# Kernel optimization log

Measured on AMD Instinct MI355X. Metric: run time of the kernel, lower is better.

## Reference

```python
import jax, jax.numpy as jnp
import numpy as np

B, NB, NS = 2048, 64, 16          # batch, boxes per tree, symmetry ops per tree
BOX, SYM, F, H = 12, 8, 512, 1024  # boxSize, symmetrySize, featureSize, hiddenSize


def _ops_seq():
    # valid shift-reduce program: shift two leaves, reduce, then (shift, reduce)
    # for the remaining leaves, then apply NS symmetry ops to the root.
    ops = [0, 0, 1]
    for _ in range(NB - 2):
        ops += [0, 1]
    ops += [2] * NS
    return np.array(ops, dtype=np.int64)


def setup_inputs():
    key = jax.random.key(0)
    ks = jax.random.split(key, 12)
    def n(k, shape, s):
        return jax.random.normal(k, shape, dtype=jnp.float32) * s
    return {
        "inputStacks": n(ks[0], (B, NB, BOX), 1.0),
        "symmetryStacks": n(ks[1], (B, NS, SYM), 1.0),
        "operations": jnp.tile(jnp.asarray(_ops_seq())[None, None, :], (B, 1, 1)),
        # BoxEncoder
        "Wb": n(ks[2], (F, BOX), BOX ** -0.5), "bb": jnp.zeros((F,), jnp.float32),
        # AdjEncoder (right linear has no bias, as in the torch module)
        "Wl": n(ks[3], (H, F), F ** -0.5), "bl": jnp.zeros((H,), jnp.float32),
        "Wr": n(ks[4], (H, F), F ** -0.5),
        "Ws": n(ks[5], (F, H), H ** -0.5), "bs": jnp.zeros((F,), jnp.float32),
        # SymEncoder
        "Sl": n(ks[6], (H, F), F ** -0.5), "sbl": jnp.zeros((H,), jnp.float32),
        "Sr": n(ks[7], (H, SYM), SYM ** -0.5), "sbr": jnp.zeros((H,), jnp.float32),
        "Ss": n(ks[8], (F, H), H ** -0.5), "sbs": jnp.zeros((F,), jnp.float32),
    }


def _forward(inputStacks, symmetryStacks, Wb, bb, Wl, bl, Wr, Ws, bs,
             Sl, sbl, Sr, sbr, Ss, sbs, ops_np):
    boxes = jnp.tanh(inputStacks @ Wb.T + bb)  # [B, NB, F]  BoxEncoder
    Bn, nb, f = boxes.shape
    # static max stack depth from the (constant) op schedule
    depth, maxd = 0, 1
    for op in ops_np:
        depth += 1 if op == 0 else (-1 if op == 1 else 0)
        maxd = max(maxd, depth)
    stack = jnp.zeros((Bn, maxd, f), boxes.dtype)
    sp, bp, symp = 0, nb, symmetryStacks.shape[1]
    for op in ops_np:  # same program for every batch element -> fully batched steps
        if op == 0:  # shift: buffers pop from the end (torch list.pop())
            bp -= 1
            stack = stack.at[:, sp].set(boxes[:, bp])
            sp += 1
        elif op == 1:  # adjacency reduce: pop right then left, push result
            left, right = stack[:, sp - 2], stack[:, sp - 1]
            h = jnp.tanh(left @ Wl.T + bl + right @ Wr.T)
            out = jnp.tanh(h @ Ws.T + bs)
            sp -= 1
            stack = stack.at[:, sp - 1].set(out)
        else:  # op == 2: symmetry reduce (pop feature + pop sym param, push)
            symp -= 1
            h = jnp.tanh(stack[:, sp - 1] @ Sl.T + sbl
                         + symmetryStacks[:, symp] @ Sr.T + sbr)
            out = jnp.tanh(h @ Ss.T + sbs)
            stack = stack.at[:, sp - 1].set(out)
    return stack[:, sp - 1]  # [B, F] root codes


def reference(inputStacks, symmetryStacks, operations, Wb, bb, Wl, bl, Wr, Ws, bs,
              Sl, sbl, Sr, sbr, Ss, sbs):
    ops_np = np.asarray(operations)[0, 0]  # identical program across the batch
    return _forward(inputStacks, symmetryStacks, Wb, bb, Wl, bl, Wr, Ws, bs,
                    Sl, sbl, Sr, sbr, Ss, sbs, ops_np)
```

## Files before the change

### kernel.cpp

```cpp
#include <hip/hip_runtime.h>
#include <cmath>

using u16 = unsigned short;
using u32 = unsigned int;
using bf16x8 = __attribute__((ext_vector_type(8))) __bf16;
using f32x4 = __attribute__((ext_vector_type(4))) float;

__device__ __forceinline__ u16 f2bf(float f) {
  union { float f; u32 i; } x; x.f = f;
  u32 r = x.i + 0x7FFFu + ((x.i >> 16) & 1u);
  return (u16)(r >> 16);
}
__device__ __forceinline__ float bf2f(u16 u) {
  union { u32 i; float f; } x; x.i = (u32)u << 16; return x.f;
}

__global__ void cvt_bf16(const float* __restrict__ src, u16* __restrict__ dst, int n) {
  int i = (blockIdx.x * 256 + threadIdx.x) * 8;
  if (i + 8 <= n) {
    float4 a = *(const float4*)(src + i), b = *(const float4*)(src + i + 4);
    u16 t[8] = {f2bf(a.x), f2bf(a.y), f2bf(a.z), f2bf(a.w),
                f2bf(b.x), f2bf(b.y), f2bf(b.z), f2bf(b.w)};
    *(uint4*)(dst + i) = *(uint4*)t;
  }
}

__global__ __launch_bounds__(256) void box_all_v2(const float* __restrict__ inp,
    const float* __restrict__ Wb, const float* __restrict__ bb, u16* __restrict__ boxes) {
  int b = blockIdx.x, t = threadIdx.x;
  __shared__ float sin_[64][12];
  for (int idx = t; idx < 768; idx += 256) sin_[idx / 12][idx % 12] = inp[(long)b * 768 + idx];
  const int f0 = t * 2;
  float w0[12], w1[12];
#pragma unroll
  for (int q = 0; q < 12; ++q) { w0[q] = Wb[f0 * 12 + q]; w1[q] = Wb[(f0 + 1) * 12 + q]; }
  float b0 = bb[f0], b1 = bb[f0 + 1];
  __syncthreads();
  for (int i = 0; i < 64; ++i) {
    float a0 = b0, a1 = b1;
#pragma unroll
    for (int q = 0; q < 12; ++q) { float x = sin_[i][q]; a0 += x * w0[q]; a1 += x * w1[q]; }
    u32 pk = (u32)f2bf(tanhf(a0)) | ((u32)f2bf(tanhf(a1)) << 16);
    *(u32*)&boxes[(((long)b * 64 + i) * 512) + f0] = pk;
  }
}

__global__ void box_one_kernel(const float* __restrict__ inp, const float* __restrict__ Wb,
                               const float* __restrict__ bb, int bp, u16* __restrict__ outBox) {
  int b = blockIdx.x;
  int f = threadIdx.x;
  __shared__ float s_in[12];
  if (f < 12) s_in[f] = inp[((long)b * 64 + bp) * 12 + f];
  __syncthreads();
  float a = bb[f];
#pragma unroll
  for (int q = 0; q < 12; ++q) a += s_in[q] * Wb[f * 12 + q];
  outBox[(long)b * 512 + f] = f2bf(tanhf(a));
}

__global__ __launch_bounds__(256) void gemm64(
    const u16* __restrict__ A1, int lda1,
    const u16* __restrict__ W1b, const float* __restrict__ W1f, int K1,
    const u16* __restrict__ A2, int lda2,
    const u16* __restrict__ W2b, const float* __restrict__ W2f, int K2,
    const float* __restrict__ bias,
    const u16* __restrict__ Radd, long ldr,
    const float* __restrict__ symS, const float* __restrict__ Srw, const float* __restrict__ sbr,
    int doTanh, int outMode, long ldRout,
    u16* __restrict__ Cb, float* __restrict__ Cf, int N) {
  __shared__ u16 As[64][72];
  __shared__ u16 Bs[64][72];
  const int tid = threadIdx.x;
  const int lane = tid & 63, w = tid >> 6;
  const int wr = w >> 1, wc = w & 1;
  const int quad = lane >> 4, l16 = lane & 15;
  const int m0 = blockIdx.y * 64, n0 = blockIdx.x * 64;
  const int srow = tid >> 2, scol = (tid & 3) * 16;

  f32x4 acc[2][2];
#pragma unroll
  for (int i = 0; i < 2; ++i)
#pragma unroll
    for (int j = 0; j < 2; ++j) acc[i][j] = (f32x4){0.f, 0.f, 0.f, 0.f};

#pragma unroll
  for (int pair = 0; pair < 2; ++pair) {
    const u16* A = pair ? A2 : A1;
    const u16* Wb_ = pair ? W2b : W1b;
    const float* Wf_ = pair ? W2f : W1f;
    const int lda = pair ? lda2 : lda1;
    const int K = pair ? K2 : K1;
    if (K == 0) continue;
    for (int k0 = 0; k0 < K; k0 += 64) {
      const u16* ap = &A[(long)(m0 + srow) * lda + k0 + scol];
      uint4 av0 = *(const uint4*)ap;
      uint4 av1 = *(const uint4*)(ap + 8);
      uint4 bv0, bv1;
      if (Wb_) {
        const u16* wp = &Wb_[(long)(n0 + srow) * K + k0 + scol];
        bv0 = *(const uint4*)wp;
        bv1 = *(const uint4*)(wp + 8);
      } else {
        const float* wp = &Wf_[(long)(n0 + srow) * K + k0 + scol];
        u16 t[16];
#pragma unroll
        for (int q = 0; q < 16; ++q) t[q] = f2bf(wp[q]);
        bv0 = ((uint4*)t)[0];
        bv1 = ((uint4*)t)[1];
      }
      __syncthreads();
      *(uint4*)&As[srow][scol] = av0;
      *(uint4*)&As[srow][scol + 8] = av1;
      *(uint4*)&Bs[srow][scol] = bv0;
      *(uint4*)&Bs[srow][scol + 8] = bv1;
      __syncthreads();
      bf16x8 af[2][2], bfv[2][2];
#pragma unroll
      for (int kk = 0; kk < 2; ++kk) {
#pragma unroll
        for (int i = 0; i < 2; ++i)
          af[i][kk] = *(const bf16x8*)&As[wr * 32 + i * 16 + l16][kk * 32 + quad * 8];
#pragma unroll
        for (int j = 0; j < 2; ++j)
          bfv[j][kk] = *(const bf16x8*)&Bs[wc * 32 + j * 16 + l16][kk * 32 + quad * 8];
      }
#pragma unroll
      for (int kk = 0; kk < 2; ++kk)
#pragma unroll
        for (int i = 0; i < 2; ++i)
#pragma unroll
          for (int j = 0; j < 2; ++j)
            acc[i][j] = __builtin_amdgcn_mfma_f32_16x16x32_bf16(af[i][kk], bfv[j][kk], acc[i][j], 0, 0, 0);
    }
  }

#pragma unroll
  for (int j = 0; j < 2; ++j) {
    const int n = n0 + wc * 32 + j * 16 + l16;
    float bn = bias ? bias[n] : 0.0f;
    float srn[8];
    if (symS) {
      bn += sbr[n];
#pragma unroll
      for (int q = 0; q < 8; ++q) srn[q] = Srw[n * 8 + q];
    }
#pragma unroll
    for (int i = 0; i < 2; ++i) {
#pragma unroll
      for (int r = 0; r < 4; ++r) {
        const int m = m0 + wr * 32 + i * 16 + quad * 4 + r;
        float v = acc[i][j][r] + bn;
        if (Radd) v += bf2f(Radd[(long)m * ldr + n]);
        if (symS) {
#pragma unroll
          for (int q = 0; q < 8; ++q) v += symS[(long)m * 128 + q] * srn[q];
        }
        if (doTanh) v = tanhf(v);
        if (outMode == 0) Cb[(long)m * N + n] = f2bf(v);
        else if (outMode == 1) Cf[(long)m * N + n] = v;
        else {
          int ii = m & 63;
          if (ii != 63) Cb[(long)ii * ldRout + (long)(m >> 6) * N + n] = f2bf(v);
        }
      }
    }
  }
}

extern "C" void kernel_launch(void* const* d_in, const int* in_sizes, int n_in,
                              void* d_out, int out_size, void* d_ws, size_t ws_size,
                              hipStream_t stream) {
  const float* inp = (const float*)d_in[0];
  const float* sym = (const float*)d_in[1];
  const float* Wb  = (const float*)d_in[3];
  const float* bb  = (const float*)d_in[4];
  const float* Wl  = (const float*)d_in[5];
  const float* bl  = (const float*)d_in[6];
  const float* Wr  = (const float*)d_in[7];
  const float* Ws  = (const float*)d_in[8];
  const float* bs  = (const float*)d_in[9];
  const float* Sl  = (const float*)d_in[10];
  const float* sbl = (const float*)d_in[11];
  const float* Sr  = (const float*)d_in[12];
  const float* sbr = (const float*)d_in[13];
  const float* Ss  = (const float*)d_in[14];
  const float* sbs = (const float*)d_in[15];

  const long B = 2048, NB = 64, F = 512, H = 1024;
  const long WE = 524288;
  u16* ws = (u16*)d_ws;

  const size_t szW = 5 * WE * 2, szBoxes = (size_t)B * NB * F * 2, szR = (size_t)63 * B * H * 2;
  const size_t szH = (size_t)B * H * 2, szAcc = (size_t)B * F * 2;
  const size_t needT1 = szW + szBoxes + szR + szH + szAcc;
  const size_t needT2 = szW + szBoxes + szH + szAcc;
  const size_t needT3 = szBoxes + szH + szAcc;
  int tier = (ws_size >= needT1) ? 1 : (ws_size >= needT2) ? 2 : (ws_size >= needT3) ? 3 : 4;

  dim3 blk(256);
  dim3 gH(16, 32), gP(8, 32), gR(16, 2048);

  u16 *WlB = nullptr, *WrB = nullptr, *WsB = nullptr, *SlB = nullptr, *SsB = nullptr;
  const float *WlF = Wl, *WrF = Wr, *WsF = Ws, *SlF = Sl, *SsF = Ss;
  u16* p = ws;
  if (tier <= 2) {
    WlB = p; WrB = p + WE; WsB = p + 2 * WE; SlB = p + 3 * WE; SsB = p + 4 * WE;
    p += 5 * WE;
    cvt_bf16<<<WE / 2048, blk, 0, stream>>>(Wl, WlB, (int)WE);
    cvt_bf16<<<WE / 2048, blk, 0, stream>>>(Wr, WrB, (int)WE);
    cvt_bf16<<<WE / 2048, blk, 0, stream>>>(Ws, WsB, (int)WE);
    cvt_bf16<<<WE / 2048, blk, 0, stream>>>(Sl, SlB, (int)WE);
    cvt_bf16<<<WE / 2048, blk, 0, stream>>>(Ss, SsB, (int)WE);
    WlF = WrF = WsF = SlF = SsF = nullptr;
  }

  u16 *accBuf, *hBuf;
  if (tier <= 3) {
    u16* boxes = p;
    p += B * NB * F;
    u16* Rbuf = nullptr;
    if (tier == 1) { Rbuf = p; p += 63 * B * H; }
    hBuf = p; p += B * H;
    accBuf = p;
    box_all_v2<<<B, blk, 0, stream>>>(inp, Wb, bb, boxes);
    if (tier == 1) {
      gemm64<<<gR, blk, 0, stream>>>(boxes, 512, WrB, WrF, 512,
                                     nullptr, 0, nullptr, nullptr, 0,
                                     nullptr, nullptr, 0, nullptr, nullptr, nullptr,
                                     0, 2, B * H, Rbuf, nullptr, 1024);
    }
    const u16* curA = boxes + 63 * 512;
    int curLda = (int)(NB * F);
    for (int bp = 62; bp >= 0; --bp) {
      if (tier == 1) {
        gemm64<<<gH, blk, 0, stream>>>(curA, curLda, WlB, WlF, 512,
                                       nullptr, 0, nullptr, nullptr, 0,
                                       bl, Rbuf + (long)bp * B * H, 1024,
                                       nullptr, nullptr, nullptr, 1, 0, 0, hBuf, nullptr, 1024);
      } else {
        gemm64<<<gH, blk, 0, stream>>>(curA, curLda, WlB, WlF, 512,
                                       boxes + (long)bp * 512, (int)(NB * F), WrB, WrF, 512,
                                       bl, nullptr, 0, nullptr, nullptr, nullptr,
                                       1, 0, 0, hBuf, nullptr, 1024);
      }
      gemm64<<<gP, blk, 0, stream>>>(hBuf, 1024, WsB, WsF, 1024,
                                     nullptr, 0, nullptr, nullptr, 0,
                                     bs, nullptr, 0, nullptr, nullptr, nullptr,
                                     1, 0, 0, accBuf, nullptr, 512);
      curA = accBuf;
      curLda = 512;
    }
  } else {
    u16* box63 = ws;
    u16* boxCur = box63 + B * F;
    hBuf = boxCur + B * F;
    accBuf = hBuf + B * H;
    box_one_kernel<<<B, 512, 0, stream>>>(inp, Wb, bb, 63, box63);
    const u16* curA = box63;
    int curLda = 512;
    for (int bp = 62; bp >= 0; --bp) {
      box_one_kernel<<<B, 512, 0, stream>>>(inp, Wb, bb, bp, boxCur);
      gemm64<<<gH, blk, 0, stream>>>(curA, curLda, nullptr, Wl, 512,
                                     boxCur, 512, nullptr, Wr, 512,
                                     bl, nullptr, 0, nullptr, nullptr, nullptr,
                                     1, 0, 0, hBuf, nullptr, 1024);
      gemm64<<<gP, blk, 0, stream>>>(hBuf, 1024, nullptr, Ws, 1024,
                                     nullptr, 0, nullptr, nullptr, 0,
                                     bs, nullptr, 0, nullptr, nullptr, nullptr,
                                     1, 0, 0, accBuf, nullptr, 512);
      curA = accBuf;
      curLda = 512;
    }
  }

  for (int symp = 15; symp >= 0; --symp) {
    gemm64<<<gH, blk, 0, stream>>>(accBuf, 512, SlB, SlF, 512,
                                   nullptr, 0, nullptr, nullptr, 0,
                                   sbl, nullptr, 0, sym + symp * 8, Sr, sbr,
                                   1, 0, 0, hBuf, nullptr, 1024);
    int om = (symp == 0) ? 1 : 0;
    gemm64<<<gP, blk, 0, stream>>>(hBuf, 1024, SsB, SsF, 1024,
                                   nullptr, 0, nullptr, nullptr, 0,
                                   sbs, nullptr, 0, nullptr, nullptr, nullptr,
                                   1, om, 0, accBuf, (float*)d_out, 512);
  }
  (void)in_sizes; (void)n_in; (void)out_size;
}
```

Baseline: 2.847 ms.

## Fuse sequential tree reduction and symmetry chain into one persistent kernel

Replaces roughly 160 per-step GEMM launches with one persistent chain_kernel. Each block owns 16 batch rows and keeps its activations in LDS across all 79 adjacency and symmetry steps, streaming bf16 weights from global/L2. It also adds a time-major box layout, a dedicated 128x128 GEMM that uses global_load_lds to precompute all right-child products, and an exp-based fast tanh. The trade-off is that only 128 blocks are launched and every step re-reads the full weights per block, which leans on L2 bandwidth; the fast tanh also slightly changes numerics.

```diff
diff --git a/kernel.cpp b/kernel.cpp
--- a/kernel.cpp
+++ b/kernel.cpp
@@ -13,6 +13,14 @@
 }
 __device__ __forceinline__ float bf2f(u16 u) {
   union { u32 i; float f; } x; x.i = (u32)u << 16; return x.f;
+}
+__device__ __forceinline__ float fast_tanh(float x) {
+  float e = __expf(2.0f * x);
+  return 1.0f - 2.0f / (e + 1.0f);
+}
+__device__ __forceinline__ void load_lds16(const u16* g, u16* l) {
+  __builtin_amdgcn_global_load_lds((const __attribute__((address_space(1))) u32*)g,
+                                   (__attribute__((address_space(3))) u32*)l, 16, 0, 0);
 }
 
 __global__ void cvt_bf16(const float* __restrict__ src, u16* __restrict__ dst, int n) {
@@ -25,6 +33,220 @@
   }
 }
 
+__global__ __launch_bounds__(256) void box_allT(const float* __restrict__ inp,
+    const float* __restrict__ Wb, const float* __restrict__ bb, u16* __restrict__ boxesT) {
+  int b = blockIdx.x, t = threadIdx.x;
+  __shared__ float sin_[64][12];
+  for (int idx = t; idx < 768; idx += 256) sin_[idx / 12][idx % 12] = inp[(long)b * 768 + idx];
+  int f0 = (t & 127) * 4, hf = t >> 7;
+  float w[4][12], bz[4];
+#pragma unroll
+  for (int r = 0; r < 4; ++r) {
+    bz[r] = bb[f0 + r];
+#pragma unroll
+    for (int q = 0; q < 12; ++q) w[r][q] = Wb[(f0 + r) * 12 + q];
+  }
+  __syncthreads();
+  for (int i = hf; i < 64; i += 2) {
+    float a[4] = {bz[0], bz[1], bz[2], bz[3]};
+#pragma unroll
+    for (int q = 0; q < 12; ++q) {
+      float x = sin_[i][q];
+#pragma unroll
+      for (int r = 0; r < 4; ++r) a[r] += x * w[r][q];
+    }
+    u16 p[4];
+#pragma unroll
+    for (int r = 0; r < 4; ++r) p[r] = f2bf(fast_tanh(a[r]));
+    *(uint2*)&boxesT[((long)i * 2048 + b) * 512 + f0] = *(uint2*)p;
+  }
+}
+
+__global__ __launch_bounds__(256, 2) void gemm_R(const u16* __restrict__ A,
+                                                 const u16* __restrict__ W,
+                                                 u16* __restrict__ R) {
+  __shared__ u16 smem[8192];
+  const int tid = threadIdx.x, lane = tid & 63, w = tid >> 6;
+  const int wr = w >> 1, wc = w & 1, q = lane >> 4, l16 = lane & 15;
+  const long m0 = (long)blockIdx.y * 128;
+  const int n0 = blockIdx.x * 128;
+  f32x4 C[4][4];
+#pragma unroll
+  for (int i = 0; i < 4; ++i)
+#pragma unroll
+    for (int j = 0; j < 4; ++j) C[i][j] = (f32x4){0.f, 0.f, 0.f, 0.f};
+
+  for (int k0 = 0; k0 < 512; k0 += 32) {
+    __syncthreads();
+#pragma unroll
+    for (int jj = 0; jj < 2; ++jj) {
+      int c = jj * 256 + w * 64;
+      int ch = c + lane;
+      load_lds16(&A[(m0 + (ch >> 2)) * 512 + k0 + (ch & 3) * 8], &smem[0] + c * 8);
+      load_lds16(&W[((long)(n0 + (ch >> 2))) * 512 + k0 + (ch & 3) * 8], &smem[4096] + c * 8);
+    }
+    __syncthreads();
+    bf16x8 af[4], bfv[4];
+#pragma unroll
+    for (int i = 0; i < 4; ++i) af[i] = *(const bf16x8*)&smem[(wr * 64 + i * 16 + l16) * 32 + q * 8];
+#pragma unroll
+    for (int j = 0; j < 4; ++j) bfv[j] = *(const bf16x8*)&smem[4096 + (wc * 64 + j * 16 + l16) * 32 + q * 8];
+#pragma unroll
+    for (int i = 0; i < 4; ++i)
+#pragma unroll
+      for (int j = 0; j < 4; ++j)
+        C[i][j] = __builtin_amdgcn_mfma_f32_16x16x32_bf16(af[i], bfv[j], C[i][j], 0, 0, 0);
+  }
+  for (int hv = 0; hv < 2; ++hv) {
+    __syncthreads();
+    if (wc == hv) {
+#pragma unroll
+      for (int i = 0; i < 4; ++i)
+#pragma unroll
+        for (int j = 0; j < 4; ++j)
+#pragma unroll
+          for (int r = 0; r < 4; ++r)
+            smem[(wr * 64 + i * 16 + q * 4 + r) * 64 + j * 16 + l16] = f2bf(C[i][j][r]);
+    }
+    __syncthreads();
+    u16* dst = R + (m0 + (tid >> 1)) * 1024 + n0 + hv * 64 + (tid & 1) * 32;
+    const u16* s = &smem[(tid >> 1) * 64 + (tid & 1) * 32];
+#pragma unroll
+    for (int v = 0; v < 4; ++v) ((uint4*)dst)[v] = ((const uint4*)s)[v];
+  }
+}
+
+__global__ __launch_bounds__(256, 1) void chain_kernel(
+    const u16* __restrict__ boxesT, const u16* __restrict__ Rbuf,
+    const u16* __restrict__ Wl, const u16* __restrict__ Ws,
+    const u16* __restrict__ Sl, const u16* __restrict__ Ss,
+    const float* __restrict__ bl, const float* __restrict__ bs,
+    const float* __restrict__ sbl, const float* __restrict__ sbr,
+    const float* __restrict__ sbs, const float* __restrict__ SrF,
+    const float* __restrict__ sym, float* __restrict__ outF) {
+  __shared__ u16 sA[16][520];
+  __shared__ u16 sH[16][1032];
+  __shared__ float sSym[16][8];
+
+  const int tid = threadIdx.x, lane = tid & 63, w = tid >> 6;
+  const int q = lane >> 4, l16 = lane & 15;
+  const int m0 = blockIdx.x * 16;
+
+  {
+    const u16* src = boxesT + ((long)63 * 2048 + m0) * 512;
+    int o = tid * 32, r = o >> 9, c = o & 511;
+#pragma unroll
+    for (int v = 0; v < 4; ++v)
+      *(uint4*)&sA[r][c + v * 8] = *(const uint4*)&src[(long)r * 512 + c + v * 8];
+  }
+  __syncthreads();
+
+  for (int t = 0; t < 79; ++t) {
+    const bool symPhase = (t >= 63);
+    const int bp = 62 - t;
+    if (symPhase) {
+      int symp = 15 - (t - 63);
+      if (tid < 128) sSym[tid >> 3][tid & 7] = sym[((long)(m0 + (tid >> 3)) * 16 + symp) * 8 + (tid & 7)];
+      __syncthreads();
+    }
+    const u16* WL = symPhase ? Sl : Wl;
+    u16 rv0[8][4], rv1[8][4];
+    if (!symPhase) {
+      const u16* rbase = Rbuf + ((long)bp * 2048 + m0) * 1024;
+#pragma unroll
+      for (int np = 0; np < 8; ++np) {
+        int nb = w * 256 + np * 32 + l16;
+#pragma unroll
+        for (int r = 0; r < 4; ++r) {
+          rv0[np][r] = rbase[(long)(q * 4 + r) * 1024 + nb];
+          rv1[np][r] = rbase[(long)(q * 4 + r) * 1024 + nb + 16];
+        }
+      }
+    }
+    bf16x8 Af[16];
+#pragma unroll
+    for (int s = 0; s < 16; ++s) Af[s] = *(const bf16x8*)&sA[l16][s * 32 + q * 8];
+    float symv[4][8];
+    if (symPhase) {
+#pragma unroll
+      for (int r = 0; r < 4; ++r)
+#pragma unroll
+        for (int k = 0; k < 8; ++k) symv[r][k] = sSym[q * 4 + r][k];
+    }
+    for (int np = 0; np < 8; ++np) {
+      int n0 = w * 256 + np * 32;
+      f32x4 C0 = {0.f, 0.f, 0.f, 0.f}, C1 = {0.f, 0.f, 0.f, 0.f};
+      const u16* w0 = WL + (long)(n0 + l16) * 512 + q * 8;
+      const u16* w1 = w0 + 16 * 512;
+#pragma unroll 8
+      for (int s = 0; s < 16; ++s) {
+        bf16x8 b0 = *(const bf16x8*)(w0 + s * 32);
+        bf16x8 b1 = *(const bf16x8*)(w1 + s * 32);
+        C0 = __builtin_amdgcn_mfma_f32_16x16x32_bf16(Af[s], b0, C0, 0, 0, 0);
+        C1 = __builtin_amdgcn_mfma_f32_16x16x32_bf16(Af[s], b1, C1, 0, 0, 0);
+      }
+      int n0b = n0 + l16, n1b = n0 + 16 + l16;
+      float bn0, bn1, sr0[8], sr1[8];
+      if (!symPhase) { bn0 = bl[n0b]; bn1 = bl[n1b]; }
+      else {
+        bn0 = sbl[n0b] + sbr[n0b]; bn1 = sbl[n1b] + sbr[n1b];
+        *(float4*)&sr0[0] = *(const float4*)&SrF[(long)n0b * 8];
+        *(float4*)&sr0[4] = *(const float4*)&SrF[(long)n0b * 8 + 4];
+        *(float4*)&sr1[0] = *(const float4*)&SrF[(long)n1b * 8];
+        *(float4*)&sr1[4] = *(const float4*)&SrF[(long)n1b * 8 + 4];
+      }
+#pragma unroll
+      for (int r = 0; r < 4; ++r) {
+        int m = q * 4 + r;
+        float v0 = C0[r] + bn0;
+        float v1 = C1[r] + bn1;
+        if (!symPhase) { v0 += bf2f(rv0[np][r]); v1 += bf2f(rv1[np][r]); }
+        else {
+#pragma unroll
+          for (int k = 0; k < 8; ++k) { v0 += symv[r][k] * sr0[k]; v1 += symv[r][k] * sr1[k]; }
+        }
+        sH[m][n0b] = f2bf(fast_tanh(v0));
+        sH[m][n1b] = f2bf(fast_tanh(v1));
+      }
+    }
+    __syncthreads();
+    const u16* WP = symPhase ? Ss : Ws;
+    const float* b2 = symPhase ? sbs : bs;
+    bf16x8 Hf[32];
+#pragma unroll
+    for (int s = 0; s < 32; ++s) Hf[s] = *(const bf16x8*)&sH[l16][s * 32 + q * 8];
+    const bool last = (t == 78);
+    for (int fp = 0; fp < 4; ++fp) {
+      int f0 = w * 128 + fp * 32;
+      f32x4 C0 = {0.f, 0.f, 0.f, 0.f}, C1 = {0.f, 0.f, 0.f, 0.f};
+      const u16* w0 = WP + (long)(f0 + l16) * 1024 + q * 8;
+      const u16* w1 = w0 + 16 * 1024;
+#pragma unroll 8
+      for (int s = 0; s < 32; ++s) {
+        bf16x8 b0 = *(const bf16x8*)(w0 + s * 32);
+        bf16x8 b1 = *(const bf16x8*)(w1 + s * 32);
+        C0 = __builtin_amdgcn_mfma_f32_16x16x32_bf16(Hf[s], b0, C0, 0, 0, 0);
+        C1 = __builtin_amdgcn_mfma_f32_16x16x32_bf16(Hf[s], b1, C1, 0, 0, 0);
+      }
+      int f0b = f0 + l16, f1b = f0 + 16 + l16;
+      float bn0 = b2[f0b], bn1 = b2[f1b];
+#pragma unroll
+      for (int r = 0; r < 4; ++r) {
+        int m = q * 4 + r;
+        float a0 = fast_tanh(C0[r] + bn0);
+        float a1 = fast_tanh(C1[r] + bn1);
+        sA[m][f0b] = f2bf(a0);
+        sA[m][f1b] = f2bf(a1);
+        if (last) {
+          outF[(long)(m0 + m) * 512 + f0b] = a0;
+          outF[(long)(m0 + m) * 512 + f1b] = a1;
+        }
+      }
+    }
+    __syncthreads();
+  }
+}
+
 __global__ __launch_bounds__(256) void box_all_v2(const float* __restrict__ inp,
     const float* __restrict__ Wb, const float* __restrict__ bb, u16* __restrict__ boxes) {
   int b = blockIdx.x, t = threadIdx.x;
@@ -40,22 +262,9 @@
     float a0 = b0, a1 = b1;
 #pragma unroll
     for (int q = 0; q < 12; ++q) { float x = sin_[i][q]; a0 += x * w0[q]; a1 += x * w1[q]; }
-    u32 pk = (u32)f2bf(tanhf(a0)) | ((u32)f2bf(tanhf(a1)) << 16);
+    u32 pk = (u32)f2bf(fast_tanh(a0)) | ((u32)f2bf(fast_tanh(a1)) << 16);
     *(u32*)&boxes[(((long)b * 64 + i) * 512) + f0] = pk;
   }
-}
-
-__global__ void box_one_kernel(const float* __restrict__ inp, const float* __restrict__ Wb,
-                               const float* __restrict__ bb, int bp, u16* __restrict__ outBox) {
-  int b = blockIdx.x;
-  int f = threadIdx.x;
-  __shared__ float s_in[12];
-  if (f < 12) s_in[f] = inp[((long)b * 64 + bp) * 12 + f];
-  __syncthreads();
-  float a = bb[f];
-#pragma unroll
-  for (int q = 0; q < 12; ++q) a += s_in[q] * Wb[f * 12 + q];
-  outBox[(long)b * 512 + f] = f2bf(tanhf(a));
 }
 
 __global__ __launch_bounds__(256) void gemm64(
@@ -64,9 +273,8 @@
     const u16* __restrict__ A2, int lda2,
     const u16* __restrict__ W2b, const float* __restrict__ W2f, int K2,
     const float* __restrict__ bias,
-    const u16* __restrict__ Radd, long ldr,
     const float* __restrict__ symS, const float* __restrict__ Srw, const float* __restrict__ sbr,
-    int doTanh, int outMode, long ldRout,
+    int doTanh, int outMode,
     u16* __restrict__ Cb, float* __restrict__ Cf, int N) {
   __shared__ u16 As[64][72];
   __shared__ u16 Bs[64][72];
@@ -76,13 +284,11 @@
   const int quad = lane >> 4, l16 = lane & 15;
   const int m0 = blockIdx.y * 64, n0 = blockIdx.x * 64;
   const int srow = tid >> 2, scol = (tid & 3) * 16;
-
   f32x4 acc[2][2];
 #pragma unroll
   for (int i = 0; i < 2; ++i)
 #pragma unroll
     for (int j = 0; j < 2; ++j) acc[i][j] = (f32x4){0.f, 0.f, 0.f, 0.f};
-
 #pragma unroll
   for (int pair = 0; pair < 2; ++pair) {
     const u16* A = pair ? A2 : A1;
@@ -102,11 +308,11 @@
         bv1 = *(const uint4*)(wp + 8);
       } else {
         const float* wp = &Wf_[(long)(n0 + srow) * K + k0 + scol];
-        u16 t[16];
-#pragma unroll
-        for (int q = 0; q < 16; ++q) t[q] = f2bf(wp[q]);
-        bv0 = ((uint4*)t)[0];
-        bv1 = ((uint4*)t)[1];
+        u16 tv[16];
+#pragma unroll
+        for (int qq = 0; qq < 16; ++qq) tv[qq] = f2bf(wp[qq]);
+        bv0 = ((uint4*)tv)[0];
+        bv1 = ((uint4*)tv)[1];
       }
       __syncthreads();
       *(uint4*)&As[srow][scol] = av0;
@@ -133,7 +339,6 @@
             acc[i][j] = __builtin_amdgcn_mfma_f32_16x16x32_bf16(af[i][kk], bfv[j][kk], acc[i][j], 0, 0, 0);
     }
   }
-
 #pragma unroll
   for (int j = 0; j < 2; ++j) {
     const int n = n0 + wc * 32 + j * 16 + l16;
@@ -142,7 +347,7 @@
     if (symS) {
       bn += sbr[n];
 #pragma unroll
-      for (int q = 0; q < 8; ++q) srn[q] = Srw[n * 8 + q];
+      for (int qq = 0; qq < 8; ++qq) srn[qq] = Srw[n * 8 + qq];
     }
 #pragma unroll
     for (int i = 0; i < 2; ++i) {
@@ -150,18 +355,13 @@
       for (int r = 0; r < 4; ++r) {
         const int m = m0 + wr * 32 + i * 16 + quad * 4 + r;
         float v = acc[i][j][r] + bn;
-        if (Radd) v += bf2f(Radd[(long)m * ldr + n]);
         if (symS) {
 #pragma unroll
-          for (int q = 0; q < 8; ++q) v += symS[(long)m * 128 + q] * srn[q];
+          for (int qq = 0; qq < 8; ++qq) v += symS[(long)m * 128 + qq] * srn[qq];
         }
-        if (doTanh) v = tanhf(v);
+        if (doTanh) v = fast_tanh(v);
         if (outMode == 0) Cb[(long)m * N + n] = f2bf(v);
-        else if (outMode == 1) Cf[(long)m * N + n] = v;
-        else {
-          int ii = m & 63;
-          if (ii != 63) Cb[(long)ii * ldRout + (long)(m >> 6) * N + n] = f2bf(v);
-        }
+        else Cf[(long)m * N + n] = v;
       }
     }
   }
@@ -189,100 +389,73 @@
   const long B = 2048, NB = 64, F = 512, H = 1024;
   const long WE = 524288;
   u16* ws = (u16*)d_ws;
-
-  const size_t szW = 5 * WE * 2, szBoxes = (size_t)B * NB * F * 2, szR = (size_t)63 * B * H * 2;
-  const size_t szH = (size_t)B * H * 2, szAcc = (size_t)B * F * 2;
-  const size_t needT1 = szW + szBoxes + szR + szH + szAcc;
-  const size_t needT2 = szW + szBoxes + szH + szAcc;
-  const size_t needT3 = szBoxes + szH + szAcc;
-  int tier = (ws_size >= needT1) ? 1 : (ws_size >= needT2) ? 2 : (ws_size >= needT3) ? 3 : 4;
-
   dim3 blk(256);
-  dim3 gH(16, 32), gP(8, 32), gR(16, 2048);
-
-  u16 *WlB = nullptr, *WrB = nullptr, *WsB = nullptr, *SlB = nullptr, *SsB = nullptr;
-  const float *WlF = Wl, *WrF = Wr, *WsF = Ws, *SlF = Sl, *SsF = Ss;
-  u16* p = ws;
-  if (tier <= 2) {
-    WlB = p; WrB = p + WE; WsB = p + 2 * WE; SlB = p + 3 * WE; SsB = p + 4 * WE;
-    p += 5 * WE;
+
+  const size_t needNew = ((size_t)5 * WE + (size_t)64 * B * F + (size_t)63 * B * H) * 2;
+
+  if (ws_size >= needNew) {
+    u16* WlB = ws;
+    u16* WrB = WlB + WE;
+    u16* WsB = WrB + WE;
+    u16* SlB = WsB + WE;
+    u16* SsB = SlB + WE;
+    u16* boxesT = SsB + WE;
+    u16* Rbuf = boxesT + 64 * B * F;
+
     cvt_bf16<<<WE / 2048, blk, 0, stream>>>(Wl, WlB, (int)WE);
     cvt_bf16<<<WE / 2048, blk, 0, stream>>>(Wr, WrB, (int)WE);
     cvt_bf16<<<WE / 2048, blk, 0, stream>>>(Ws, WsB, (int)WE);
     cvt_bf16<<<WE / 2048, blk, 0, stream>>>(Sl, SlB, (int)WE);
     cvt_bf16<<<WE / 2048, blk, 0, stream>>>(Ss, SsB, (int)WE);
-    WlF = WrF = WsF = SlF = SsF = nullptr;
-  }
-
-  u16 *accBuf, *hBuf;
-  if (tier <= 3) {
+    box_allT<<<B, blk, 0, stream>>>(inp, Wb, bb, boxesT);
+    gemm_R<<<dim3(8, 1008), blk, 0, stream>>>(boxesT, WrB, Rbuf);
+    chain_kernel<<<128, blk, 0, stream>>>(boxesT, Rbuf, WlB, WsB, SlB, SsB,
+                                          bl, bs, sbl, sbr, sbs, Sr, sym, (float*)d_out);
+  } else {
+    dim3 gH(16, 32), gP(8, 32);
+    const size_t szW = 5 * WE * 2, szBoxes = (size_t)B * NB * F * 2;
+    const size_t szH = (size_t)B * H * 2, szAcc = (size_t)B * F * 2;
+    const size_t needT2 = szW + szBoxes + szH + szAcc;
+    const size_t needT3 = szBoxes + szH + szAcc;
+    int tier = (ws_size >= needT2) ? 2 : (ws_size >= needT3) ? 3 : 4;
+    u16 *WlB = nullptr, *WrB = nullptr, *WsB = nullptr, *SlB = nullptr, *SsB = nullptr;
+    const float *WlF = Wl, *WrF = Wr, *WsF = Ws, *SlF = Sl, *SsF = Ss;
+    u16* p = ws;
+    if (tier == 2) {
+      WlB = p; WrB = p + WE; WsB = p + 2 * WE; SlB = p + 3 * WE; SsB = p + 4 * WE;
+      p += 5 * WE;
+      cvt_bf16<<<WE / 2048, blk, 0, stream>>>(Wl, WlB, (int)WE);
+      cvt_bf16<<<WE / 2048, blk, 0, stream>>>(Wr, WrB, (int)WE);
+      cvt_bf16<<<WE / 2048, blk, 0, stream>>>(Ws, WsB, (int)WE);
+      cvt_bf16<<<WE / 2048, blk, 0, stream>>>(Sl, SlB, (int)WE);
+      cvt_bf16<<<WE / 2048, blk, 0, stream>>>(Ss, SsB, (int)WE);
+      WlF = WrF = WsF = SlF = SsF = nullptr;
+    }
     u16* boxes = p;
     p += B * NB * F;
-    u16* Rbuf = nullptr;
-    if (tier == 1) { Rbuf = p; p += 63 * B * H; }
-    hBuf = p; p += B * H;
-    accBuf = p;
+    u16* hBuf = p; p += B * H;
+    u16* accBuf = p;
     box_all_v2<<<B, blk, 0, stream>>>(inp, Wb, bb, boxes);
-    if (tier == 1) {
-      gemm64<<<gR, blk, 0, stream>>>(boxes, 512, WrB, WrF, 512,
-                                     nullptr, 0, nullptr, nullptr, 0,
-                                     nullptr, nullptr, 0, nullptr, nullptr, nullptr,
-                                     0, 2, B * H, Rbuf, nullptr, 1024);
-    }
     const u16* curA = boxes + 63 * 512;
     int curLda = (int)(NB * F);
     for (int bp = 62; bp >= 0; --bp) {
-      if (tier == 1) {
-        gemm64<<<gH, blk, 0, stream>>>(curA, curLda, WlB, WlF, 512,
-                                       nullptr, 0, nullptr, nullptr, 0,
-                                       bl, Rbuf + (long)bp * B * H, 1024,
-                                       nullptr, nullptr, nullptr, 1, 0, 0, hBuf, nullptr, 1024);
-      } else {
-        gemm64<<<gH, blk, 0, stream>>>(curA, curLda, WlB, WlF, 512,
-                                       boxes + (long)bp * 512, (int)(NB * F), WrB, WrF, 512,
-                                       bl, nullptr, 0, nullptr, nullptr, nullptr,
-                                       1, 0, 0, hBuf, nullptr, 1024);
-      }
+      gemm64<<<gH, blk, 0, stream>>>(curA, curLda, WlB, WlF, 512,
+                                     boxes + (long)bp * 512, (int)(NB * F), WrB, WrF, 512,
+                                     bl, nullptr, nullptr, nullptr, 1, 0, hBuf, nullptr, 1024);
       gemm64<<<gP, blk, 0, stream>>>(hBuf, 1024, WsB, WsF, 1024,
                                      nullptr, 0, nullptr, nullptr, 0,
-                                     bs, nullptr, 0, nullptr, nullptr, nullptr,
-                                     1, 0, 0, accBuf, nullptr, 512);
-      curA = accBuf;
-      curLda = 512;
-    }
-  } else {
-    u16* box63 = ws;
-    u16* boxCur = box63 + B * F;
-    hBuf = boxCur + B * F;
-    accBuf = hBuf + B * H;
-    box_one_kernel<<<B, 512, 0, stream>>>(inp, Wb, bb, 63, box63);
-    const u16* curA = box63;
-    int curLda = 512;
-    for (int bp = 62; bp >= 0; --bp) {
-      box_one_kernel<<<B, 512, 0, stream>>>(inp, Wb, bb, bp, boxCur);
-      gemm64<<<gH, blk, 0, stream>>>(curA, curLda, nullptr, Wl, 512,
-                                     boxCur, 512, nullptr, Wr, 512,
-                                     bl, nullptr, 0, nullptr, nullptr, nullptr,
-                                     1, 0, 0, hBuf, nullptr, 1024);
-      gemm64<<<gP, blk, 0, stream>>>(hBuf, 1024, nullptr, Ws, 1024,
+                                     bs, nullptr, nullptr, nullptr, 1, 0, accBuf, nullptr, 512);
+      curA = accBuf; curLda = 512;
+    }
+    for (int symp = 15; symp >= 0; --symp) {
+      gemm64<<<gH, blk, 0, stream>>>(accBuf, 512, SlB, SlF, 512,
                                      nullptr, 0, nullptr, nullptr, 0,
-                                     bs, nullptr, 0, nullptr, nullptr, nullptr,
-                                     1, 0, 0, accBuf, nullptr, 512);
-      curA = accBuf;
-      curLda = 512;
-    }
-  }
-
-  for (int symp = 15; symp >= 0; --symp) {
-    gemm64<<<gH, blk, 0, stream>>>(accBuf, 512, SlB, SlF, 512,
-                                   nullptr, 0, nullptr, nullptr, 0,
-                                   sbl, nullptr, 0, sym + symp * 8, Sr, sbr,
-                                   1, 0, 0, hBuf, nullptr, 1024);
-    int om = (symp == 0) ? 1 : 0;
-    gemm64<<<gP, blk, 0, stream>>>(hBuf, 1024, SsB, SsF, 1024,
-                                   nullptr, 0, nullptr, nullptr, 0,
-                                   sbs, nullptr, 0, nullptr, nullptr, nullptr,
-                                   1, om, 0, accBuf, (float*)d_out, 512);
+                                     sbl, sym + symp * 8, Sr, sbr, 1, 0, hBuf, nullptr, 1024);
+      int om = (symp == 0) ? 1 : 0;
+      gemm64<<<gP, blk, 0, stream>>>(hBuf, 1024, SsB, SsF, 1024,
+                                     nullptr, 0, nullptr, nullptr, 0,
+                                     sbs, nullptr, nullptr, nullptr, 1, om, accBuf, (float*)d_out, 512);
+    }
   }
   (void)in_sizes; (void)n_in; (void)out_size;
 }
```

Measured after the change: 2.444 ms. -14.1%, faster.
